# Kernel optimization log

Hardware: AMD Instinct MI355X
Metric: run time of the kernel (lower is better)

## Reference

```python
import jax, jax.numpy as jnp
import numpy as np

LOSS_WEIGHT = 1.0


def setup_inputs() -> dict:
    key = jax.random.key(0)
    k1, k2 = jax.random.split(key)
    H = W = 1024
    n = H * W  # 1,048,576 vertices
    # structured grid triangulation -> m = 2*(H-1)*(W-1) = 2,092,098 faces
    base = (np.arange(H - 1)[:, None] * W + np.arange(W - 1)[None, :]).ravel()
    v00, v01, v10, v11 = base, base + 1, base + W, base + W + 1
    f1 = np.stack([v00, v01, v11], axis=1)
    f2 = np.stack([v00, v11, v10], axis=1)
    face = jnp.asarray(np.concatenate([f1, f2], axis=0), dtype=jnp.int32)
    vert_s = jax.random.normal(k1, (n, 3), dtype=jnp.float32)
    vert_t = vert_s + 0.05 * jax.random.normal(k2, (n, 3), dtype=jnp.float32)
    return {"vert_s": vert_s, "vert_t": vert_t, "face": face}


def reference(vert_s, vert_t, face):
    n = vert_s.shape[0]
    diff = vert_t - vert_s  # (n,3)
    i0, i1, i2 = face[:, 0], face[:, 1], face[:, 2]
    V0, V1, V2 = vert_s[i0], vert_s[i1], vert_s[i2]  # (m,3)
    v21, v02, v10 = V2 - V1, V0 - V2, V1 - V0
    nvec = jnp.cross(v21, v02)  # (m,3) unnormalized face normal
    dblA = jnp.linalg.norm(nvec, axis=1)  # (m,) double area
    u = nvec / dblA[:, None]  # unit normal

    def eperp(v):
        c = jnp.cross(u, v)
        scale = jnp.linalg.norm(v, axis=1) / (dblA * jnp.linalg.norm(c, axis=1))
        return c * scale[:, None]

    e02 = eperp(v02)  # (m,3): cols are the x/y/z gradient-operator coefficients
    e10 = eperp(v10)
    area = 0.5 * dblA  # (m,)

    # Sparse G structure (dense to_dense sums duplicate i0 entries):
    #   row f of G_a: +e02[f,a] at i1, +e10[f,a] at i2, -(e02+e10)[f,a] at i0
    d10 = diff[i1] - diff[i0]  # (m,3)
    d20 = diff[i2] - diff[i0]  # (m,3)
    # g[f,a,:] = (G_a @ diff)[f];  aw = area-diag weighted
    g = e02[:, :, None] * d10[:, None, :] + e10[:, :, None] * d20[:, None, :]  # (m,3,3)
    aw = area[:, None, None] * g  # (m,3,3)

    idx = jnp.concatenate([i1, i2, i0])  # (3m,)
    coef = jnp.concatenate([e02, e10, -(e02 + e10)], axis=0)  # (3m,3)
    aw3 = jnp.concatenate([aw, aw, aw], axis=0)  # (3m,3,3)

    def GaT_area_Gb_diff(a, b):
        # G_a.T @ diag(area) @ G_b @ diff  via scatter-add over faces -> (n,3)
        vals = coef[:, a, None] * aw3[:, b, :]  # (3m,3)
        return jax.ops.segment_sum(vals, idx, num_segments=n)

    Hxx = GaT_area_Gb_diff(0, 0)
    Hyy = GaT_area_Gb_diff(1, 1)
    Hzz = GaT_area_Gb_diff(2, 2)
    Hxy = GaT_area_Gb_diff(0, 1)
    Hxz = GaT_area_Gb_diff(0, 2)
    Hyz = GaT_area_Gb_diff(1, 2)

    Hdf = jnp.mean(Hxx**2 + Hyy**2 + Hzz**2 + 2.0 * (Hxy**2 + Hxz**2 + Hyz**2))
    return Hdf * LOSS_WEIGHT
```

## Files before the change

kernel.cpp:

```cpp
#include <hip/hip_runtime.h>
#include <math.h>


struct FS { float ex, ey, ez, fx, fy, fz, area; };

__device__ __forceinline__ FS fsetup(float3 V0, float3 V1, float3 V2)
{
    float v21x = V2.x - V1.x, v21y = V2.y - V1.y, v21z = V2.z - V1.z;
    float v02x = V0.x - V2.x, v02y = V0.y - V2.y, v02z = V0.z - V2.z;
    float v10x = V1.x - V0.x, v10y = V1.y - V0.y, v10z = V1.z - V0.z;
    float nx = v21y * v02z - v21z * v02y;
    float ny = v21z * v02x - v21x * v02z;
    float nz = v21x * v02y - v21y * v02x;
    float A2 = nx * nx + ny * ny + nz * nz;
    float inv = __builtin_amdgcn_rcpf(A2);
    FS s;
    s.ex = (ny * v02z - nz * v02y) * inv;
    s.ey = (nz * v02x - nx * v02z) * inv;
    s.ez = (nx * v02y - ny * v02x) * inv;
    s.fx = (ny * v10z - nz * v10y) * inv;
    s.fy = (nz * v10x - nx * v10z) * inv;
    s.fz = (nx * v10y - ny * v10x) * inv;
    s.area = 0.5f * sqrtf(A2);
    return s;
}

template <int ROLE>
__device__ __forceinline__ void fcontrib(const FS f, float3 D0, float3 D1, float3 D2,
                                         float acc[6][3])
{
    float d1[3] = {D1.x - D0.x, D1.y - D0.y, D1.z - D0.z};
    float d2[3] = {D2.x - D0.x, D2.y - D0.y, D2.z - D0.z};
    float e[3] = {f.ex, f.ey, f.ez};
    float h[3] = {f.fx, f.fy, f.fz};
    float g[3][3];
#pragma unroll
    for (int b = 0; b < 3; ++b)
#pragma unroll
        for (int c = 0; c < 3; ++c) g[b][c] = e[b] * d1[c] + h[b] * d2[c];
    float ka[3];
#pragma unroll
    for (int a = 0; a < 3; ++a) {
        float k = (ROLE == 1) ? e[a] : (ROLE == 2) ? h[a] : -(e[a] + h[a]);
        ka[a] = f.area * k;
    }
    const int pa[6] = {0, 1, 2, 0, 0, 1};
    const int pb[6] = {0, 1, 2, 1, 2, 2};
#pragma unroll
    for (int p = 0; p < 6; ++p)
#pragma unroll
        for (int c = 0; c < 3; ++c) acc[p][c] += ka[pa[p]] * g[pb[p]][c];
}

__device__ __forceinline__ float sq_acc(const float acc[6][3])
{
    float s1 = 0.0f, s2 = 0.0f;
#pragma unroll
    for (int p = 0; p < 3; ++p)
#pragma unroll
        for (int c = 0; c < 3; ++c) s1 += acc[p][c] * acc[p][c];
#pragma unroll
    for (int p = 3; p < 6; ++p)
#pragma unroll
        for (int c = 0; c < 3; ++c) s2 += acc[p][c] * acc[p][c];
    return s1 + 2.0f * s2;
}

__device__ __forceinline__ float3 d3(float3 t, float3 v)
{
    return make_float3(t.x - v.x, t.y - v.y, t.z - v.z);
}

#define MK 4

__global__ __launch_bounds__(256)
void hess_march(const float* __restrict__ vsf, const float* __restrict__ vtf,
                float* __restrict__ acc_out, int W, int H)
{
    const float3* vs = (const float3*)vsf;
    const float3* vt = (const float3*)vtf;
    const int c = blockIdx.x * blockDim.x + threadIdx.x;
    const int r0 = blockIdx.y * MK;

    float s = 0.0f;
    if (c < W) {
        const bool cp = (c < W - 1), cm = (c > 0);
        const int ccm = cm ? c - 1 : c;
        const int ccp = cp ? c + 1 : c;

        const int rowm = (r0 > 0 ? r0 - 1 : 0) * W;
        const int row0 = r0 * W;
        const int rowp = (r0 < H - 1 ? r0 + 1 : H - 1) * W;

        float3 Vdd = vs[rowm + ccm], Vu = vs[rowm + c];
        float3 Vm  = vs[row0 + ccm], V00 = vs[row0 + c], V01 = vs[row0 + ccp];
        float3 V10 = vs[rowp + c],   V11 = vs[rowp + ccp];
        float3 Ddd = d3(vt[rowm + ccm], Vdd), Du = d3(vt[rowm + c], Vu);
        float3 Dm  = d3(vt[row0 + ccm], Vm);
        float3 D00 = d3(vt[row0 + c], V00), D01 = d3(vt[row0 + ccp], V01);
        float3 D10 = d3(vt[rowp + c], V10), D11 = d3(vt[rowp + ccp], V11);

        FS F4 = fsetup(Vdd, Vu, V00);
        FS F6 = fsetup(Vu, V01, V00);

#pragma unroll
        for (int k = 0; k < MK; ++k) {
            const int r = r0 + k;
            const bool rp = (r < H - 1), rm = (r > 0);

            FS F1 = fsetup(V00, V01, V11);
            FS F2 = fsetup(V00, V11, V10);
            FS F3 = fsetup(Vm, V00, V10);
            FS F5 = fsetup(Vdd, V00, Vm);

            float acc[6][3] = {};
            if (rp && cp) {
                fcontrib<0>(F1, D00, D01, D11, acc);
                fcontrib<0>(F2, D00, D11, D10, acc);
            }
            if (rp && cm)
                fcontrib<1>(F3, Dm, D00, D10, acc);
            if (rm && cm) {
                fcontrib<2>(F4, Ddd, Du, D00, acc);
                fcontrib<1>(F5, Ddd, D00, Dm, acc);
            }
            if (rm && cp)
                fcontrib<2>(F6, Du, D01, D00, acc);
            s += sq_acc(acc);

            if (k < MK - 1) {
                const int rowa = (r + 1) * W;
                const int rowb = (r + 2 < H ? r + 2 : H - 1) * W;
                float3 nVm  = vs[rowa + ccm];
                float3 nV10 = vs[rowb + c];
                float3 nV11 = vs[rowb + ccp];
                float3 nTm  = vt[rowa + ccm];
                float3 nT10 = vt[rowb + c];
                float3 nT11 = vt[rowb + ccp];
                Vdd = Vm;  Ddd = Dm;
                Du  = D00;
                Vm  = nVm;  Dm  = d3(nTm, nVm);
                V00 = V10;  D00 = D10;
                V01 = V11;  D01 = D11;
                V10 = nV10; D10 = d3(nT10, nV10);
                V11 = nV11; D11 = d3(nT11, nV11);
                F4 = F3;  F6 = F2;
            }
        }
    }

#pragma unroll
    for (int o = 32; o > 0; o >>= 1) s += __shfl_down(s, o, 64);
    __shared__ float sm[4];
    int lane = threadIdx.x & 63, wid = threadIdx.x >> 6;
    if (lane == 0) sm[wid] = s;
    __syncthreads();
    if (threadIdx.x == 0) {
        float t = sm[0] + sm[1] + sm[2] + sm[3];
        atomicAdd(acc_out, t);
    }
}


__device__ __forceinline__ void loadP(const float3* __restrict__ vs,
                                      const float3* __restrict__ vt,
                                      int idx, float3& V, float3& D)
{
    V = vs[idx];
    D = d3(vt[idx], V);
}

__global__ void hess_gather(const float* __restrict__ vsf, const float* __restrict__ vtf,
                            float* __restrict__ acc_out, int W, int H)
{
    const float3* vs = (const float3*)vsf;
    const float3* vt = (const float3*)vtf;
    int v = blockIdx.x * blockDim.x + threadIdx.x;
    int n = W * H;
    float s = 0.0f;
    if (v < n) {
        int r = v / W;
        int c = v - r * W;
        bool rp = (r < H - 1), rm = (r >= 1), cp = (c < W - 1), cm = (c >= 1);
        float3 P00V, P00D, P01V, P01D, P11V, P11D, P10V, P10D;
        float3 PmV, PmD, PddV, PddD, PuV, PuD;
        loadP(vs, vt, v, P00V, P00D);
        loadP(vs, vt, cp ? v + 1 : v, P01V, P01D);
        loadP(vs, vt, (rp && cp) ? v + W + 1 : v, P11V, P11D);
        loadP(vs, vt, rp ? v + W : v, P10V, P10D);
        loadP(vs, vt, cm ? v - 1 : v, PmV, PmD);
        loadP(vs, vt, (rm && cm) ? v - W - 1 : v, PddV, PddD);
        loadP(vs, vt, rm ? v - W : v, PuV, PuD);
        float acc[6][3] = {};
        if (rp && cp) {
            fcontrib<0>(fsetup(P00V, P01V, P11V), P00D, P01D, P11D, acc);
            fcontrib<0>(fsetup(P00V, P11V, P10V), P00D, P11D, P10D, acc);
        }
        if (rp && cm)
            fcontrib<1>(fsetup(PmV, P00V, P10V), PmD, P00D, P10D, acc);
        if (rm && cm) {
            fcontrib<2>(fsetup(PddV, PuV, P00V), PddD, PuD, P00D, acc);
            fcontrib<1>(fsetup(PddV, P00V, PmV), PddD, P00D, PmD, acc);
        }
        if (rm && cp)
            fcontrib<2>(fsetup(PuV, P01V, P00V), PuD, P01D, P00D, acc);
        s = sq_acc(acc);
    }
#pragma unroll
    for (int o = 32; o > 0; o >>= 1) s += __shfl_down(s, o, 64);
    __shared__ float sm[4];
    int lane = threadIdx.x & 63, wid = threadIdx.x >> 6;
    if (lane == 0) sm[wid] = s;
    __syncthreads();
    if (threadIdx.x == 0) {
        float t = sm[0] + sm[1] + sm[2] + sm[3];
        atomicAdd(acc_out, t);
    }
}

__global__ void finalize(const float* __restrict__ acc, float* __restrict__ out, int n)
{
    out[0] = acc[0] / (3.0f * (float)n);
}


extern "C" void kernel_launch(void* const* d_in, const int* in_sizes, int n_in,
                              void* d_out, int out_size, void* d_ws, size_t ws_size,
                              hipStream_t stream)
{
    const float* vs = (const float*)d_in[0];
    const float* vt = (const float*)d_in[1];
    int n = in_sizes[0] / 3;
    int F = in_sizes[2] / 3;

    int W = (int)(sqrt((double)n) + 0.5);
    int H = (W > 0) ? n / W : 0;
    bool grid_ok = (W > 1) && ((long long)W * H == n) &&
                   (2LL * (W - 1) * (H - 1) == F);

    float* acc = (float*)d_ws;
    hipMemsetAsync(acc, 0, sizeof(float), stream);

    if (grid_ok && (H % MK == 0)) {
        dim3 block(256, 1, 1);
        dim3 grid((W + 255) / 256, H / MK, 1);
        hess_march<<<grid, block, 0, stream>>>(vs, vt, acc, W, H);
    } else {
        int threads = 256;
        int blocks = (n + threads - 1) / threads;
        hess_gather<<<blocks, threads, 0, stream>>>(vs, vt, acc, W, H);
    }
    finalize<<<1, 1, 0, stream>>>(acc, (float*)d_out, n);
}
```

Measured before the change: 34.61 us.

## Share column neighbours via wavefront shuffles and replace atomic reduction with partials

The marching kernel now loads only its own column's vertices and gets left and right neighbours through cross-lane shuffles, with only edge lanes issuing extra loads. This cuts redundant global and cache traffic. Next-row loads are issued before the face computation to hide latency. The single atomic accumulator, its memset and the one-thread finalize are replaced by per-block partial sums plus a 256-thread final reduction kernel. The cost is extra shuffle instructions and divergent edge-lane loads.

```diff
diff --git a/kernel.cpp b/kernel.cpp
--- a/kernel.cpp
+++ b/kernel.cpp
@@ -71,94 +71,125 @@
     return make_float3(t.x - v.x, t.y - v.y, t.z - v.z);
 }
 
+__device__ __forceinline__ float3 shfl_up3(float3 v)
+{
+    return make_float3(__shfl_up(v.x, 1, 64), __shfl_up(v.y, 1, 64),
+                       __shfl_up(v.z, 1, 64));
+}
+__device__ __forceinline__ float3 shfl_dn3(float3 v)
+{
+    return make_float3(__shfl_down(v.x, 1, 64), __shfl_down(v.y, 1, 64),
+                       __shfl_down(v.z, 1, 64));
+}
+
 #define MK 4
 
 __global__ __launch_bounds__(256)
-void hess_march(const float* __restrict__ vsf, const float* __restrict__ vtf,
-                float* __restrict__ acc_out, int W, int H)
+void hess_march2(const float* __restrict__ vsf, const float* __restrict__ vtf,
+                 float* __restrict__ partials, int W, int H)
 {
     const float3* vs = (const float3*)vsf;
     const float3* vt = (const float3*)vtf;
-    const int c = blockIdx.x * blockDim.x + threadIdx.x;
+    const int tid = threadIdx.x;
+    const int lane = tid & 63;
+    const int c = blockIdx.x * blockDim.x + tid;
+    const int cL = (c < W) ? c : W - 1;
     const int r0 = blockIdx.y * MK;
+    const bool cp = (c < W - 1), cm = (c > 0);
+    const int ccm = cm ? cL - 1 : cL;
+    const int ccp = cp ? cL + 1 : cL;
+
+    const int rowm = (r0 > 0 ? r0 - 1 : 0) * W;
+    const int row0 = r0 * W;
+    const int rowp = (r0 + 1 < H ? r0 + 1 : H - 1) * W;
+
+    float3 A = vs[rowm + cL];  float3 dA = d3(vt[rowm + cL], A);
+    float3 B = vs[row0 + cL];  float3 dB = d3(vt[row0 + cL], B);
+    float3 C = vs[rowp + cL];  float3 dC = d3(vt[rowp + cL], C);
+
+    float3 Vu = A, Du = dA;
+    float3 V00 = B, D00 = dB;
+    float3 V10 = C, D10 = dC;
+
+    float3 Vdd = shfl_up3(A), Ddd = shfl_up3(dA);
+    float3 Vm  = shfl_up3(B), Dm  = shfl_up3(dB);
+    float3 V01 = shfl_dn3(B), D01 = shfl_dn3(dB);
+    float3 V11 = shfl_dn3(C), D11 = shfl_dn3(dC);
+    if (lane == 0) {
+        float3 v = vs[rowm + ccm]; Vdd = v; Ddd = d3(vt[rowm + ccm], v);
+        v = vs[row0 + ccm]; Vm = v; Dm = d3(vt[row0 + ccm], v);
+    }
+    if (lane == 63) {
+        float3 v = vs[row0 + ccp]; V01 = v; D01 = d3(vt[row0 + ccp], v);
+        v = vs[rowp + ccp]; V11 = v; D11 = d3(vt[rowp + ccp], v);
+    }
+
+    FS F4 = fsetup(Vdd, Vu, V00);
+    FS F6 = fsetup(Vu, V01, V00);
 
     float s = 0.0f;
-    if (c < W) {
-        const bool cp = (c < W - 1), cm = (c > 0);
-        const int ccm = cm ? c - 1 : c;
-        const int ccp = cp ? c + 1 : c;
-
-        const int rowm = (r0 > 0 ? r0 - 1 : 0) * W;
-        const int row0 = r0 * W;
-        const int rowp = (r0 < H - 1 ? r0 + 1 : H - 1) * W;
-
-        float3 Vdd = vs[rowm + ccm], Vu = vs[rowm + c];
-        float3 Vm  = vs[row0 + ccm], V00 = vs[row0 + c], V01 = vs[row0 + ccp];
-        float3 V10 = vs[rowp + c],   V11 = vs[rowp + ccp];
-        float3 Ddd = d3(vt[rowm + ccm], Vdd), Du = d3(vt[rowm + c], Vu);
-        float3 Dm  = d3(vt[row0 + ccm], Vm);
-        float3 D00 = d3(vt[row0 + c], V00), D01 = d3(vt[row0 + ccp], V01);
-        float3 D10 = d3(vt[rowp + c], V10), D11 = d3(vt[rowp + ccp], V11);
-
-        FS F4 = fsetup(Vdd, Vu, V00);
-        FS F6 = fsetup(Vu, V01, V00);
-
-#pragma unroll
-        for (int k = 0; k < MK; ++k) {
-            const int r = r0 + k;
-            const bool rp = (r < H - 1), rm = (r > 0);
-
-            FS F1 = fsetup(V00, V01, V11);
-            FS F2 = fsetup(V00, V11, V10);
-            FS F3 = fsetup(Vm, V00, V10);
-            FS F5 = fsetup(Vdd, V00, Vm);
-
-            float acc[6][3] = {};
-            if (rp && cp) {
-                fcontrib<0>(F1, D00, D01, D11, acc);
-                fcontrib<0>(F2, D00, D11, D10, acc);
-            }
-            if (rp && cm)
-                fcontrib<1>(F3, Dm, D00, D10, acc);
-            if (rm && cm) {
-                fcontrib<2>(F4, Ddd, Du, D00, acc);
-                fcontrib<1>(F5, Ddd, D00, Dm, acc);
-            }
-            if (rm && cp)
-                fcontrib<2>(F6, Du, D01, D00, acc);
-            s += sq_acc(acc);
-
-            if (k < MK - 1) {
-                const int rowa = (r + 1) * W;
-                const int rowb = (r + 2 < H ? r + 2 : H - 1) * W;
-                float3 nVm  = vs[rowa + ccm];
-                float3 nV10 = vs[rowb + c];
-                float3 nV11 = vs[rowb + ccp];
-                float3 nTm  = vt[rowa + ccm];
-                float3 nT10 = vt[rowb + c];
-                float3 nT11 = vt[rowb + ccp];
-                Vdd = Vm;  Ddd = Dm;
-                Du  = D00;
-                Vm  = nVm;  Dm  = d3(nTm, nVm);
-                V00 = V10;  D00 = D10;
-                V01 = V11;  D01 = D11;
-                V10 = nV10; D10 = d3(nT10, nV10);
-                V11 = nV11; D11 = d3(nT11, nV11);
-                F4 = F3;  F6 = F2;
-            }
-        }
-    }
+#pragma unroll
+    for (int k = 0; k < MK; ++k) {
+        const int r = r0 + k;
+        const bool rp = (r < H - 1), rm = (r > 0);
+
+        float3 P2 = make_float3(0.f, 0.f, 0.f), T2 = P2;
+        float3 PmL = P2, TmL = P2, P2p = P2, T2p = P2;
+        if (k < MK - 1) {
+            const int rowa = (r + 1) * W;
+            const int rowb = (r + 2 < H ? r + 2 : H - 1) * W;
+            P2 = vs[rowb + cL];
+            T2 = vt[rowb + cL];
+            if (lane == 0)  { PmL = vs[rowa + ccm]; TmL = vt[rowa + ccm]; }
+            if (lane == 63) { P2p = vs[rowb + ccp]; T2p = vt[rowb + ccp]; }
+        }
+
+        FS F1 = fsetup(V00, V01, V11);
+        FS F2 = fsetup(V00, V11, V10);
+        FS F3 = fsetup(Vm, V00, V10);
+        FS F5 = fsetup(Vdd, V00, Vm);
+
+        float acc[6][3] = {};
+        if (rp && cp) {
+            fcontrib<0>(F1, D00, D01, D11, acc);
+            fcontrib<0>(F2, D00, D11, D10, acc);
+        }
+        if (rp && cm)
+            fcontrib<1>(F3, Dm, D00, D10, acc);
+        if (rm && cm) {
+            fcontrib<2>(F4, Ddd, Du, D00, acc);
+            fcontrib<1>(F5, Ddd, D00, Dm, acc);
+        }
+        if (rm && cp)
+            fcontrib<2>(F6, Du, D01, D00, acc);
+        s += sq_acc(acc);
+
+        if (k < MK - 1) {
+            float3 D2 = d3(T2, P2);
+            float3 nVm = shfl_up3(V10), nDm = shfl_up3(D10);
+            float3 nV11 = shfl_dn3(P2), nD11 = shfl_dn3(D2);
+            if (lane == 0)  { nVm = PmL; nDm = d3(TmL, PmL); }
+            if (lane == 63) { nV11 = P2p; nD11 = d3(T2p, P2p); }
+            Vdd = Vm;  Ddd = Dm;
+            Du  = D00;
+            Vm  = nVm;  Dm  = nDm;
+            V00 = V10;  D00 = D10;
+            V01 = V11;  D01 = D11;
+            V10 = P2;   D10 = D2;
+            V11 = nV11; D11 = nD11;
+            F4 = F3;  F6 = F2;
+        }
+    }
+    if (c >= W) s = 0.0f;
 
 #pragma unroll
     for (int o = 32; o > 0; o >>= 1) s += __shfl_down(s, o, 64);
     __shared__ float sm[4];
-    int lane = threadIdx.x & 63, wid = threadIdx.x >> 6;
+    int wid = tid >> 6;
     if (lane == 0) sm[wid] = s;
     __syncthreads();
-    if (threadIdx.x == 0) {
-        float t = sm[0] + sm[1] + sm[2] + sm[3];
-        atomicAdd(acc_out, t);
-    }
+    if (tid == 0)
+        partials[blockIdx.y * gridDim.x + blockIdx.x] = sm[0] + sm[1] + sm[2] + sm[3];
 }
 
 
@@ -171,7 +202,7 @@
 }
 
 __global__ void hess_gather(const float* __restrict__ vsf, const float* __restrict__ vtf,
-                            float* __restrict__ acc_out, int W, int H)
+                            float* __restrict__ partials, int W, int H)
 {
     const float3* vs = (const float3*)vsf;
     const float3* vt = (const float3*)vtf;
@@ -212,15 +243,23 @@
     int lane = threadIdx.x & 63, wid = threadIdx.x >> 6;
     if (lane == 0) sm[wid] = s;
     __syncthreads();
-    if (threadIdx.x == 0) {
-        float t = sm[0] + sm[1] + sm[2] + sm[3];
-        atomicAdd(acc_out, t);
-    }
-}
-
-__global__ void finalize(const float* __restrict__ acc, float* __restrict__ out, int n)
-{
-    out[0] = acc[0] / (3.0f * (float)n);
+    if (threadIdx.x == 0)
+        partials[blockIdx.x] = sm[0] + sm[1] + sm[2] + sm[3];
+}
+
+__global__ void finalize_sum(const float* __restrict__ partials, int nparts,
+                             float* __restrict__ out, int n)
+{
+    float s = 0.0f;
+    for (int i = threadIdx.x; i < nparts; i += 256) s += partials[i];
+#pragma unroll
+    for (int o = 32; o > 0; o >>= 1) s += __shfl_down(s, o, 64);
+    __shared__ float sm[4];
+    int lane = threadIdx.x & 63, wid = threadIdx.x >> 6;
+    if (lane == 0) sm[wid] = s;
+    __syncthreads();
+    if (threadIdx.x == 0)
+        out[0] = (sm[0] + sm[1] + sm[2] + sm[3]) / (3.0f * (float)n);
 }
 
 
@@ -238,17 +277,18 @@
     bool grid_ok = (W > 1) && ((long long)W * H == n) &&
                    (2LL * (W - 1) * (H - 1) == F);
 
-    float* acc = (float*)d_ws;
-    hipMemsetAsync(acc, 0, sizeof(float), stream);
+    float* partials = (float*)d_ws;
 
     if (grid_ok && (H % MK == 0)) {
         dim3 block(256, 1, 1);
         dim3 grid((W + 255) / 256, H / MK, 1);
-        hess_march<<<grid, block, 0, stream>>>(vs, vt, acc, W, H);
+        int nparts = grid.x * grid.y;
+        hess_march2<<<grid, block, 0, stream>>>(vs, vt, partials, W, H);
+        finalize_sum<<<1, 256, 0, stream>>>(partials, nparts, (float*)d_out, n);
     } else {
         int threads = 256;
         int blocks = (n + threads - 1) / threads;
-        hess_gather<<<blocks, threads, 0, stream>>>(vs, vt, acc, W, H);
-    }
-    finalize<<<1, 1, 0, stream>>>(acc, (float*)d_out, n);
-}
+        hess_gather<<<blocks, threads, 0, stream>>>(vs, vt, partials, W, H);
+        finalize_sum<<<1, 256, 0, stream>>>(partials, blocks, (float*)d_out, n);
+    }
+}
```

Result: faster. 30.85 us (-10.9%).
